# Performance work log

Hardware: AMD Instinct MI355X
Metric: run time of the kernel (lower is better)

Reference implementation:

```python
import jax, jax.numpy as jnp
import numpy as np

N = 8192
F_IN = 256
F_OUT = 256


def setup_inputs() -> dict:
    key = jax.random.key(0)
    k1, k2, k3, k4 = jax.random.split(key, 4)
    return {
        "input": jax.random.normal(k1, (N, F_IN), dtype=jnp.float32),
        "adj": jax.random.uniform(k2, (N, N), dtype=jnp.float32),
        "weight": jax.random.normal(k3, (F_IN, F_OUT), dtype=jnp.float32) * (1.0 / np.sqrt(F_OUT)),
        "bias": jax.random.normal(k4, (F_OUT,), dtype=jnp.float32) * (1.0 / np.sqrt(F_OUT)),
    }


def reference(input, adj, weight, bias):
    n = input.shape[0]
    # add_identity=True: adj <- adj + I
    a = adj + jnp.eye(n, dtype=adj.dtype)
    # D^{-1/2} as a vector; diag-matmul == row/col elementwise scaling
    d = jax.lax.rsqrt(jnp.sum(a, axis=1))  # [n]
    adj_norm = d[:, None] * a * d[None, :]  # [n, n]
    support = input @ weight                # [n, f_out]
    out = adj_norm @ support + bias         # [n, f_out]
    return out
```

## Files before the change

### kernel.cpp

```cpp
#include <hip/hip_runtime.h>
#include <stdint.h>

#define N_ROWS 8192
#define F_DIM 256
#define SPLITK 4
#define KSTRIP (N_ROWS / SPLITK)

typedef __attribute__((ext_vector_type(8))) short s16x8;
typedef __attribute__((ext_vector_type(4))) float f32x4;
typedef __attribute__((address_space(3))) uint32_t lds_u32_t;
typedef __attribute__((address_space(1))) const uint32_t gbl_u32_t;

__device__ __forceinline__ void gl_lds16(const void* g, void* l) {
    __builtin_amdgcn_global_load_lds((gbl_u32_t*)g, (lds_u32_t*)l, 16, 0, 0);
}

__device__ __forceinline__ unsigned short f2bf(float f) {
    unsigned int u = __float_as_uint(f);
    u += 0x7FFFu + ((u >> 16) & 1u);
    return (unsigned short)(u >> 16);
}
__device__ __forceinline__ float bf2f(unsigned short h) {
    return __uint_as_float(((unsigned int)h) << 16);
}
__device__ __forceinline__ s16x8 cvt8(f32x4 a, f32x4 b) {
    s16x8 r;
    r[0] = (short)f2bf(a[0]); r[1] = (short)f2bf(a[1]);
    r[2] = (short)f2bf(a[2]); r[3] = (short)f2bf(a[3]);
    r[4] = (short)f2bf(b[0]); r[5] = (short)f2bf(b[1]);
    r[6] = (short)f2bf(b[2]); r[7] = (short)f2bf(b[3]);
    return r;
}

__global__ void k_rowsum(const float* __restrict__ adj, float* __restrict__ dvec) {
    const int row = blockIdx.x;
    const float4* p = (const float4*)(adj + (size_t)row * N_ROWS);
    float s = 0.f;
#pragma unroll
    for (int i = 0; i < 8; ++i) {
        float4 v = p[threadIdx.x + i * 256];
        s += (v.x + v.y) + (v.z + v.w);
    }
#pragma unroll
    for (int off = 32; off > 0; off >>= 1) s += __shfl_down(s, off, 64);
    __shared__ float red[4];
    if ((threadIdx.x & 63) == 0) red[threadIdx.x >> 6] = s;
    __syncthreads();
    if (threadIdx.x == 0) {
        float t = red[0] + red[1] + red[2] + red[3] + 1.0f;
        dvec[row] = rsqrtf(t);
    }
}

__global__ void k_wt(const float* __restrict__ w, unsigned short* __restrict__ wt) {
    const int j = blockIdx.x, t = threadIdx.x;
    wt[j * F_DIM + t] = f2bf(w[t * F_DIM + j]);
}

__global__ __launch_bounds__(256, 2)
void k_support(const float* __restrict__ input, const unsigned short* __restrict__ wt,
               const float* __restrict__ dvec, unsigned short* __restrict__ sup) {
    __shared__ float As[128 * 32];
    __shared__ unsigned short Bs[128 * 32];
    const int tid = threadIdx.x, lane = tid & 63, wid = tid >> 6;
    const int wm = wid & 1, wn = wid >> 1;
    const int l15 = lane & 15, q4 = lane >> 4;
    const int m0 = blockIdx.x * 128, n0 = blockIdx.y * 128;

    uint32_t aoff[4], alds[4], boff[2], blds[2];
#pragma unroll
    for (int i = 0; i < 4; ++i) {
        int row = wid * 32 + i * 8 + (lane >> 3);
        aoff[i] = (uint32_t)(m0 + row) * F_DIM + (lane & 7) * 4;
        alds[i] = (uint32_t)(wid * 32 + i * 8) * 32;
    }
#pragma unroll
    for (int i = 0; i < 2; ++i) {
        int row = wid * 32 + i * 16 + (lane >> 2);
        boff[i] = (uint32_t)(n0 + row) * F_DIM + (lane & 3) * 8;
        blds[i] = (uint32_t)(wid * 32 + i * 16) * 32;
    }

    const f32x4* aptr[4];
    const s16x8* bptr[4];
#pragma unroll
    for (int a = 0; a < 4; ++a)
        aptr[a] = (const f32x4*)(As + (wm * 64 + a * 16 + l15) * 32 + q4 * 8);
#pragma unroll
    for (int b = 0; b < 4; ++b)
        bptr[b] = (const s16x8*)(Bs + (wn * 64 + b * 16 + l15) * 32 + q4 * 8);

    f32x4 acc[4][4];
#pragma unroll
    for (int a = 0; a < 4; ++a)
#pragma unroll
        for (int b = 0; b < 4; ++b) acc[a][b] = (f32x4){0.f, 0.f, 0.f, 0.f};

#pragma unroll 1
    for (int it = 0; it < F_DIM / 32; ++it) {
        __syncthreads();
#pragma unroll
        for (int i = 0; i < 4; ++i) gl_lds16(input + aoff[i], As + alds[i]);
#pragma unroll
        for (int i = 0; i < 2; ++i) gl_lds16(wt + boff[i], Bs + blds[i]);
        __syncthreads();
        s16x8 af[4];
#pragma unroll
        for (int a = 0; a < 4; ++a) af[a] = cvt8(aptr[a][0], aptr[a][1]);
#pragma unroll
        for (int b = 0; b < 4; ++b) {
            s16x8 bf = *bptr[b];
#pragma unroll
            for (int a = 0; a < 4; ++a)
                acc[a][b] = __builtin_amdgcn_mfma_f32_16x16x32_bf16(af[a], bf, acc[a][b], 0, 0, 0);
        }
#pragma unroll
        for (int i = 0; i < 4; ++i) aoff[i] += 32;
#pragma unroll
        for (int i = 0; i < 2; ++i) boff[i] += 32;
    }

#pragma unroll
    for (int a = 0; a < 4; ++a) {
        const int rbase = m0 + wm * 64 + a * 16 + q4 * 4;
        float dv[4];
#pragma unroll
        for (int r = 0; r < 4; ++r) dv[r] = dvec[rbase + r];
#pragma unroll
        for (int b = 0; b < 4; ++b) {
            const int col = n0 + wn * 64 + b * 16 + l15;
            f32x4 c = acc[a][b];
#pragma unroll
            for (int r = 0; r < 4; ++r)
                sup[(size_t)(rbase + r) * F_DIM + col] = f2bf(dv[r] * c[r]);
        }
    }
}

__global__ void k_transpose(const unsigned short* __restrict__ src,
                            unsigned short* __restrict__ dst) {
    __shared__ unsigned short t[64][65];
    const int r0 = blockIdx.x * 64, c0 = blockIdx.y * 64;
    const int lr = threadIdx.x >> 2, lc = (threadIdx.x & 3) * 16;
#pragma unroll
    for (int i = 0; i < 16; ++i)
        t[lr][lc + i] = src[(size_t)(r0 + lr) * F_DIM + c0 + lc + i];
    __syncthreads();
#pragma unroll
    for (int i = 0; i < 16; ++i)
        dst[(size_t)(c0 + lr) * N_ROWS + r0 + lc + i] = t[lc + i][lr];
}

__global__ __launch_bounds__(256, 2)
void k_main(const float* __restrict__ adj, const unsigned short* __restrict__ sup_t,
            float* __restrict__ part) {
    __shared__ float As[64 * 32];
    __shared__ unsigned short Bs[256 * 32];
    const int tid = threadIdx.x, lane = tid & 63, wid = tid >> 6;
    const int l15 = lane & 15, q4 = lane >> 4;
    const int m0 = blockIdx.x * 64;
    const int kbase = blockIdx.y * KSTRIP;

    uint32_t aoff[2], alds[2];
#pragma unroll
    for (int r = 0; r < 2; ++r) {
        int idx = r * 256 + tid;
        aoff[r] = (uint32_t)(m0 + (idx >> 3)) * N_ROWS + kbase + (idx & 7) * 4;
        alds[r] = (uint32_t)(r * 1024 + wid * 256);
    }
    uint32_t boff[4], blds[4];
#pragma unroll
    for (int r = 0; r < 4; ++r) {
        int idx = r * 256 + tid;
        boff[r] = (uint32_t)(idx >> 2) * N_ROWS + kbase + (idx & 3) * 8;
        blds[r] = (uint32_t)(r * 2048 + wid * 512);
    }

    const f32x4* aptr[4];
    const s16x8* bptr[4];
#pragma unroll
    for (int a = 0; a < 4; ++a)
        aptr[a] = (const f32x4*)(As + (a * 16 + l15) * 32 + q4 * 8);
#pragma unroll
    for (int b = 0; b < 4; ++b)
        bptr[b] = (const s16x8*)(Bs + (wid * 64 + b * 16 + l15) * 32 + q4 * 8);

    f32x4 acc[4][4];
#pragma unroll
    for (int a = 0; a < 4; ++a)
#pragma unroll
        for (int b = 0; b < 4; ++b) acc[a][b] = (f32x4){0.f, 0.f, 0.f, 0.f};

#pragma unroll 1
    for (int it = 0; it < KSTRIP / 32; ++it) {
        __syncthreads();
#pragma unroll
        for (int r = 0; r < 2; ++r) gl_lds16(adj + aoff[r], As + alds[r]);
#pragma unroll
        for (int r = 0; r < 4; ++r) gl_lds16(sup_t + boff[r], Bs + blds[r]);
        __syncthreads();
        s16x8 af[4];
#pragma unroll
        for (int a = 0; a < 4; ++a) af[a] = cvt8(aptr[a][0], aptr[a][1]);
#pragma unroll
        for (int b = 0; b < 4; ++b) {
            s16x8 bf = *bptr[b];
#pragma unroll
            for (int a = 0; a < 4; ++a)
                acc[a][b] = __builtin_amdgcn_mfma_f32_16x16x32_bf16(af[a], bf, acc[a][b], 0, 0, 0);
        }
#pragma unroll
        for (int r = 0; r < 2; ++r) aoff[r] += 32;
#pragma unroll
        for (int r = 0; r < 4; ++r) boff[r] += 32;
    }

    float* p = part + (size_t)blockIdx.y * ((size_t)N_ROWS * F_DIM);
#pragma unroll
    for (int a = 0; a < 4; ++a) {
        const int rbase = m0 + a * 16 + q4 * 4;
#pragma unroll
        for (int b = 0; b < 4; ++b) {
            const int col = wid * 64 + b * 16 + l15;
            f32x4 c = acc[a][b];
#pragma unroll
            for (int r = 0; r < 4; ++r)
                p[(size_t)(rbase + r) * F_DIM + col] = c[r];
        }
    }
}

__global__ void k_reduce(const float* __restrict__ part, const unsigned short* __restrict__ sup,
                         const float* __restrict__ dvec, const float* __restrict__ bias,
                         float* __restrict__ out) {
    const int gid = blockIdx.x * 256 + threadIdx.x;
    const int row = gid >> 6;
    const int c = (gid & 63) * 4;
    const size_t off = (size_t)row * F_DIM + c;
    const size_t PS = (size_t)N_ROWS * F_DIM;
    f32x4 v = *(const f32x4*)(part + off);
#pragma unroll
    for (int s = 1; s < SPLITK; ++s) v += *(const f32x4*)(part + s * PS + off);
    const float d = dvec[row];
    const unsigned short* sp = sup + off;
    const f32x4 bb = *(const f32x4*)(bias + c);
    f32x4 o;
#pragma unroll
    for (int r = 0; r < 4; ++r) o[r] = d * (v[r] + bf2f(sp[r])) + bb[r];
    *(f32x4*)(out + off) = o;
}

extern "C" void kernel_launch(void* const* d_in, const int* in_sizes, int n_in,
                              void* d_out, int out_size, void* d_ws, size_t ws_size,
                              hipStream_t stream) {
    const float* input  = (const float*)d_in[0];
    const float* adj    = (const float*)d_in[1];
    const float* weight = (const float*)d_in[2];
    const float* bias   = (const float*)d_in[3];
    float* out = (float*)d_out;

    char* ws = (char*)d_ws;
    float* dvec           = (float*)ws;
    unsigned short* wt    = (unsigned short*)(ws + (32 << 10));
    unsigned short* sup   = (unsigned short*)(ws + (32 << 10) + (128 << 10));
    unsigned short* sup_t = (unsigned short*)(ws + (32 << 10) + (128 << 10)
                                              + (size_t)N_ROWS * F_DIM * 2);
    float* part           = (float*)(ws + (32 << 10) + (128 << 10)
                                     + 2 * (size_t)N_ROWS * F_DIM * 2);

    k_rowsum<<<dim3(N_ROWS), dim3(256), 0, stream>>>(adj, dvec);
    k_wt<<<dim3(F_DIM), dim3(F_DIM), 0, stream>>>(weight, wt);
    k_support<<<dim3(64, 2), dim3(256), 0, stream>>>(input, wt, dvec, sup);
    k_transpose<<<dim3(128, 4), dim3(256), 0, stream>>>(sup, sup_t);
    k_main<<<dim3(128, SPLITK), dim3(256), 0, stream>>>(adj, sup_t, part);
    k_reduce<<<dim3((N_ROWS * F_DIM / 4) / 256), dim3(256), 0, stream>>>(part, sup, dvec, bias, out);
}
```

Before: 485.3 us.

## XOR-swizzle LDS tiles in GEMMs and fuse support transpose into epilogue

Applies XOR swizzling to the global-to-LDS load column groups and the matching LDS read offsets in both k_support and k_main, to remove LDS bank conflicts on the MFMA operand reads. It also removes the separate transpose kernel by having the k_support epilogue write the transposed bf16 support directly with packed 4-element stores. This saves one launch and a round trip through global memory, but the transposed stores are strided by N_ROWS and only 8 bytes wide.

```diff
diff --git a/kernel.cpp b/kernel.cpp
--- a/kernel.cpp
+++ b/kernel.cpp
@@ -7,6 +7,7 @@
 #define KSTRIP (N_ROWS / SPLITK)
 
 typedef __attribute__((ext_vector_type(8))) short s16x8;
+typedef __attribute__((ext_vector_type(4))) short s16x4;
 typedef __attribute__((ext_vector_type(4))) float f32x4;
 typedef __attribute__((address_space(3))) uint32_t lds_u32_t;
 typedef __attribute__((address_space(1))) const uint32_t gbl_u32_t;
@@ -59,7 +60,8 @@
 
 __global__ __launch_bounds__(256, 2)
 void k_support(const float* __restrict__ input, const unsigned short* __restrict__ wt,
-               const float* __restrict__ dvec, unsigned short* __restrict__ sup) {
+               const float* __restrict__ dvec, unsigned short* __restrict__ sup,
+               unsigned short* __restrict__ sup_t) {
     __shared__ float As[128 * 32];
     __shared__ unsigned short Bs[128 * 32];
     const int tid = threadIdx.x, lane = tid & 63, wid = tid >> 6;
@@ -71,24 +73,31 @@
 #pragma unroll
     for (int i = 0; i < 4; ++i) {
         int row = wid * 32 + i * 8 + (lane >> 3);
-        aoff[i] = (uint32_t)(m0 + row) * F_DIM + (lane & 7) * 4;
+        int cg = (lane & 7) ^ (lane >> 3);
+        aoff[i] = (uint32_t)(m0 + row) * F_DIM + cg * 4;
         alds[i] = (uint32_t)(wid * 32 + i * 8) * 32;
     }
 #pragma unroll
     for (int i = 0; i < 2; ++i) {
         int row = wid * 32 + i * 16 + (lane >> 2);
-        boff[i] = (uint32_t)(n0 + row) * F_DIM + (lane & 3) * 8;
+        int cg = (lane & 3) ^ ((lane >> 3) & 3);
+        boff[i] = (uint32_t)(n0 + row) * F_DIM + cg * 8;
         blds[i] = (uint32_t)(wid * 32 + i * 16) * 32;
     }
 
-    const f32x4* aptr[4];
+    const int ra7 = l15 & 7;
+    const int rb3 = (l15 >> 1) & 3;
+    const f32x4* aptr[4][2];
     const s16x8* bptr[4];
 #pragma unroll
     for (int a = 0; a < 4; ++a)
-        aptr[a] = (const f32x4*)(As + (wm * 64 + a * 16 + l15) * 32 + q4 * 8);
+#pragma unroll
+        for (int j = 0; j < 2; ++j)
+            aptr[a][j] = (const f32x4*)(As + (wm * 64 + a * 16 + l15) * 32
+                                        + (((2 * q4 + j) ^ ra7) * 4));
 #pragma unroll
     for (int b = 0; b < 4; ++b)
-        bptr[b] = (const s16x8*)(Bs + (wn * 64 + b * 16 + l15) * 32 + q4 * 8);
+        bptr[b] = (const s16x8*)(Bs + (wn * 64 + b * 16 + l15) * 32 + ((q4 ^ rb3) * 8));
 
     f32x4 acc[4][4];
 #pragma unroll
@@ -106,7 +115,7 @@
         __syncthreads();
         s16x8 af[4];
 #pragma unroll
-        for (int a = 0; a < 4; ++a) af[a] = cvt8(aptr[a][0], aptr[a][1]);
+        for (int a = 0; a < 4; ++a) af[a] = cvt8(aptr[a][0][0], aptr[a][1][0]);
 #pragma unroll
         for (int b = 0; b < 4; ++b) {
             s16x8 bf = *bptr[b];
@@ -130,25 +139,16 @@
         for (int b = 0; b < 4; ++b) {
             const int col = n0 + wn * 64 + b * 16 + l15;
             f32x4 c = acc[a][b];
-#pragma unroll
-            for (int r = 0; r < 4; ++r)
-                sup[(size_t)(rbase + r) * F_DIM + col] = f2bf(dv[r] * c[r]);
-        }
-    }
-}
-
-__global__ void k_transpose(const unsigned short* __restrict__ src,
-                            unsigned short* __restrict__ dst) {
-    __shared__ unsigned short t[64][65];
-    const int r0 = blockIdx.x * 64, c0 = blockIdx.y * 64;
-    const int lr = threadIdx.x >> 2, lc = (threadIdx.x & 3) * 16;
-#pragma unroll
-    for (int i = 0; i < 16; ++i)
-        t[lr][lc + i] = src[(size_t)(r0 + lr) * F_DIM + c0 + lc + i];
-    __syncthreads();
-#pragma unroll
-    for (int i = 0; i < 16; ++i)
-        dst[(size_t)(c0 + lr) * N_ROWS + r0 + lc + i] = t[lc + i][lr];
+            s16x4 pk;
+#pragma unroll
+            for (int r = 0; r < 4; ++r) {
+                unsigned short h = f2bf(dv[r] * c[r]);
+                pk[r] = (short)h;
+                sup[(size_t)(rbase + r) * F_DIM + col] = h;
+            }
+            *(s16x4*)(sup_t + (size_t)col * N_ROWS + rbase) = pk;
+        }
+    }
 }
 
 __global__ __launch_bounds__(256, 2)
@@ -165,25 +165,33 @@
 #pragma unroll
     for (int r = 0; r < 2; ++r) {
         int idx = r * 256 + tid;
-        aoff[r] = (uint32_t)(m0 + (idx >> 3)) * N_ROWS + kbase + (idx & 7) * 4;
+        int row = idx >> 3;
+        int cg = (idx & 7) ^ (row & 7);
+        aoff[r] = (uint32_t)(m0 + row) * N_ROWS + kbase + cg * 4;
         alds[r] = (uint32_t)(r * 1024 + wid * 256);
     }
     uint32_t boff[4], blds[4];
 #pragma unroll
     for (int r = 0; r < 4; ++r) {
         int idx = r * 256 + tid;
-        boff[r] = (uint32_t)(idx >> 2) * N_ROWS + kbase + (idx & 3) * 8;
+        int row = idx >> 2;
+        int cg = (idx & 3) ^ ((row >> 1) & 3);
+        boff[r] = (uint32_t)row * N_ROWS + kbase + cg * 8;
         blds[r] = (uint32_t)(r * 2048 + wid * 512);
     }
 
-    const f32x4* aptr[4];
+    const int ra7 = l15 & 7;
+    const int rb3 = (l15 >> 1) & 3;
+    const f32x4* aptr[4][2];
     const s16x8* bptr[4];
 #pragma unroll
     for (int a = 0; a < 4; ++a)
-        aptr[a] = (const f32x4*)(As + (a * 16 + l15) * 32 + q4 * 8);
+#pragma unroll
+        for (int j = 0; j < 2; ++j)
+            aptr[a][j] = (const f32x4*)(As + (a * 16 + l15) * 32 + (((2 * q4 + j) ^ ra7) * 4));
 #pragma unroll
     for (int b = 0; b < 4; ++b)
-        bptr[b] = (const s16x8*)(Bs + (wid * 64 + b * 16 + l15) * 32 + q4 * 8);
+        bptr[b] = (const s16x8*)(Bs + (wid * 64 + b * 16 + l15) * 32 + ((q4 ^ rb3) * 8));
 
     f32x4 acc[4][4];
 #pragma unroll
@@ -201,7 +209,7 @@
         __syncthreads();
         s16x8 af[4];
 #pragma unroll
-        for (int a = 0; a < 4; ++a) af[a] = cvt8(aptr[a][0], aptr[a][1]);
+        for (int a = 0; a < 4; ++a) af[a] = cvt8(aptr[a][0][0], aptr[a][1][0]);
 #pragma unroll
         for (int b = 0; b < 4; ++b) {
             s16x8 bf = *bptr[b];
@@ -270,8 +278,7 @@
 
     k_rowsum<<<dim3(N_ROWS), dim3(256), 0, stream>>>(adj, dvec);
     k_wt<<<dim3(F_DIM), dim3(F_DIM), 0, stream>>>(weight, wt);
-    k_support<<<dim3(64, 2), dim3(256), 0, stream>>>(input, wt, dvec, sup);
-    k_transpose<<<dim3(128, 4), dim3(256), 0, stream>>>(sup, sup_t);
+    k_support<<<dim3(64, 2), dim3(256), 0, stream>>>(input, wt, dvec, sup, sup_t);
     k_main<<<dim3(128, SPLITK), dim3(256), 0, stream>>>(adj, sup_t, part);
     k_reduce<<<dim3((N_ROWS * F_DIM / 4) / 256), dim3(256), 0, stream>>>(part, sup, dvec, bias, out);
 }
```

New measurement: 483.3 us. About the same (-0.4%).
